# Kernel tuning notes

Measured on AMD Instinct MI355X. Metric: run time of the kernel, lower is better.

Reference implementation:

```python
import jax, jax.numpy as jnp
import numpy as np

N_NODES = 80000
N_EDGES = 1280000
D_NODE = 128
D_EDGE = 32
HID = 64
OUT = 32
EPS_GEN = 1e-7
EPS_BN = 1e-5


def _lin_init(key, fan_in, fan_out):
    return (jax.random.normal(key, (fan_in, fan_out), jnp.float32) / np.sqrt(fan_in))


def setup_inputs() -> dict:
    key = jax.random.key(0)
    ks = jax.random.split(key, 20)
    inp = {
        "x": jax.random.normal(ks[0], (N_NODES, D_NODE), jnp.float32),
        "edge_index": jax.random.randint(ks[1], (2, N_EDGES), 0, N_NODES, jnp.int32),
        "edge_attr": jax.random.normal(ks[2], (N_EDGES, D_EDGE), jnp.float32),
        # encoders
        "node_W": _lin_init(ks[3], D_NODE, HID), "node_b": jnp.zeros((HID,), jnp.float32),
        "edge_W": _lin_init(ks[4], D_EDGE, HID), "edge_b": jnp.zeros((HID,), jnp.float32),
        # GENConv layer 1 MLP: [HID -> 2HID (bias=False)] -> BN -> ReLU -> [2HID -> HID (bias=False)]
        "c1_W1": _lin_init(ks[5], HID, 2 * HID), "c1_g": jnp.ones((2 * HID,), jnp.float32), "c1_be": jnp.zeros((2 * HID,), jnp.float32), "c1_W2": _lin_init(ks[6], 2 * HID, HID),
        # GENConv layer 2
        "c2_W1": _lin_init(ks[7], HID, 2 * HID), "c2_g": jnp.ones((2 * HID,), jnp.float32), "c2_be": jnp.zeros((2 * HID,), jnp.float32), "c2_W2": _lin_init(ks[8], 2 * HID, HID),
        # edge update linears on concat(3*HID)
        "l1_W": _lin_init(ks[9], 3 * HID, HID), "l1_b": jnp.zeros((HID,), jnp.float32),
        "l2_W": _lin_init(ks[10], 3 * HID, OUT), "l2_b": jnp.zeros((OUT,), jnp.float32),
    }
    return inp


def _scatter_softmax_agg(msg, dst, n_nodes):
    # SoftmaxAggregation with t=1: per-destination, per-feature softmax weights
    m = jax.ops.segment_max(msg, dst, num_segments=n_nodes)  # [N, H]
    m = jnp.where(jnp.isfinite(m), m, 0.0)                   # nodes w/o in-edges
    ex = jnp.exp(msg - m[dst])                               # [E, H]
    denom = jax.ops.segment_sum(ex, dst, num_segments=n_nodes)
    alpha = ex / (denom[dst] + 1e-16)
    return jax.ops.segment_sum(msg * alpha, dst, num_segments=n_nodes)


def _batchnorm(h, gamma, beta):
    mu = jnp.mean(h, axis=0)
    var = jnp.var(h, axis=0)
    return (h - mu) * jax.lax.rsqrt(var + EPS_BN) * gamma + beta


def _genconv(x, src, dst, edge_attr, W1, g, be, W2):
    msg = jax.nn.relu(x[src] + edge_attr) + EPS_GEN          # [E, HID]
    agg = _scatter_softmax_agg(msg, dst, x.shape[0])         # [N, HID]
    h = agg + x
    h = jax.nn.relu(_batchnorm(h @ W1, g, be))
    return h @ W2


def reference(x, edge_index, edge_attr, node_W, node_b, edge_W, edge_b,
              c1_W1, c1_g, c1_be, c1_W2, c2_W1, c2_g, c2_be, c2_W2,
              l1_W, l1_b, l2_W, l2_b):
    src, dst = edge_index[0], edge_index[1]
    ea = edge_attr @ edge_W + edge_b                          # [E, HID]
    h = x @ node_W + node_b                                   # [N, HID]

    convs = [(c1_W1, c1_g, c1_be, c1_W2), (c2_W1, c2_g, c2_be, c2_W2)]
    lins = [(l1_W, l1_b), (l2_W, l2_b)]
    for (W1, g, be, W2), (lW, lb) in zip(convs, lins):
        h = jax.nn.relu(_genconv(h, src, dst, ea, W1, g, be, W2))
        # dropout is identity in eval mode
        ef = jnp.concatenate([h[src], ea, h[dst]], axis=-1)   # [E, 3*HID]
        ea = ef @ lW + lb
    return h, ea
```

## Files before the change

### kernel.cpp

```cpp
#include <hip/hip_runtime.h>
#include <hip/hip_bf16.h>

#define N_NODES 80000
#define N_EDGES 1280000
constexpr int DN = 128;
constexpr int DE = 32;
constexpr int H  = 64;
constexpr int H2 = 128;
constexpr int CSTRIDE = 32;
constexpr float EPS_GEN = 1e-7f;
constexpr float EPS_BN  = 1e-5f;

typedef _Float16 f16x8 __attribute__((ext_vector_type(8)));
typedef _Float16 f16x4 __attribute__((ext_vector_type(4)));
typedef float f32x4 __attribute__((ext_vector_type(4)));

__device__ __forceinline__ void atomAddF(float* p, float v) {
  __hip_atomic_fetch_add(p, v, __ATOMIC_RELAXED, __HIP_MEMORY_SCOPE_AGENT);
}

struct PrepDesc { const float* W; _Float16* img; int K; int OC; int blkStart; };
struct PrepAll { PrepDesc d[8]; };

__global__ void k_prep_all(PrepAll P) {
  int b = blockIdx.x;
  int i = 0;
#pragma unroll
  for (int t = 1; t < 8; ++t)
    if (P.d[t].blkStart <= b) i = t;
  const PrepDesc D = P.d[i];
  int idx = (b - D.blkStart) * 256 + threadIdx.x;
  if (idx >= D.K * D.OC) return;
  int nslabK = D.K >> 5;
  int j = idx & 7, m16 = (idx >> 3) & 15, kg = (idx >> 7) & 3;
  int slab = idx >> 9;
  int kk = slab % nslabK, n2 = slab / nslabK;
  int k = kk * 32 + kg * 8 + j, n = n2 * 16 + m16;
  D.img[idx] = (_Float16)D.W[k * D.OC + n];
}

template <int K, int OC, bool IN16, bool AFFINE, bool BIAS,
          bool RELU_OUT, bool OUT16, bool OUT32, bool SCATOUT, bool STATS>
__global__ __launch_bounds__(256) void k_dense(
    const void* __restrict__ Ain, const _Float16* __restrict__ wimg,
    const float* __restrict__ bias, const float* __restrict__ sums,
    const float* __restrict__ g, const float* __restrict__ be,
    const int* __restrict__ posmap,
    _Float16* __restrict__ out16, float* __restrict__ out32,
    float* __restrict__ sums_out) {
  constexpr int NK = K / 32, NF = OC / 16;
  __shared__ float sSC[AFFINE ? H2 : 1], sSH[AFFINE ? H2 : 1];
  __shared__ float sStat[STATS ? 1024 : 1];
  const int tid = threadIdx.x, wv = tid >> 6, lane = tid & 63;
  const int m16 = lane & 15, kg = lane >> 4;
  const int rowbase = blockIdx.x * 64 + wv * 16;
  if constexpr (AFFINE) {
    for (int i = tid; i < H2; i += 256) {
      float mu  = sums[i] * (1.0f / N_NODES);
      float var = sums[H2 + i] * (1.0f / N_NODES) - mu * mu;
      float sc  = rsqrtf(var + EPS_BN) * g[i];
      sSC[i] = sc;
      sSH[i] = be[i] - mu * sc;
    }
    __syncthreads();
  }
  const int arow = rowbase + m16;
  f32x4 acc[NF];
#pragma unroll
  for (int n2 = 0; n2 < NF; ++n2) {
    float bv = BIAS ? bias[n2 * 16 + m16] : 0.0f;
    acc[n2] = (f32x4){bv, bv, bv, bv};
  }
  const _Float16* wp = wimg + (size_t)lane * 8;
#pragma unroll
  for (int kk = 0; kk < NK; ++kk) {
    f16x8 a;
    if constexpr (IN16) {
      const _Float16* ap = (const _Float16*)Ain + (size_t)arow * K + kg * 8 + kk * 32;
      a = *(const f16x8*)ap;
      if constexpr (AFFINE) {
#pragma unroll
        for (int j = 0; j < 8; ++j) {
          int f = kg * 8 + kk * 32 + j;
          float v = fmaxf(fmaf((float)a[j], sSC[f], sSH[f]), 0.0f);
          a[j] = (_Float16)v;
        }
      }
    } else {
      const float* ap = (const float*)Ain + (size_t)arow * K + kg * 8 + kk * 32;
      float4 v0 = *(const float4*)ap;
      float4 v1 = *(const float4*)(ap + 4);
      a = (f16x8){(_Float16)v0.x, (_Float16)v0.y, (_Float16)v0.z, (_Float16)v0.w,
                  (_Float16)v1.x, (_Float16)v1.y, (_Float16)v1.z, (_Float16)v1.w};
    }
#pragma unroll
    for (int n2 = 0; n2 < NF; ++n2) {
      f16x8 bb = *(const f16x8*)(wp + ((size_t)(n2 * NK + kk) << 9));
      acc[n2] = __builtin_amdgcn_mfma_f32_16x16x32_f16(a, bb, acc[n2], 0, 0, 0);
    }
  }
#pragma unroll
  for (int n2 = 0; n2 < NF; ++n2)
#pragma unroll
    for (int r = 0; r < 4; ++r) {
      float o = acc[n2][r];
      if constexpr (RELU_OUT) o = fmaxf(o, 0.0f);
      int orow = rowbase + kg * 4 + r;
      if constexpr (SCATOUT) orow = posmap[orow];
      size_t oi = (size_t)orow * OC + n2 * 16 + m16;
      if constexpr (OUT16) out16[oi] = (_Float16)o;
      if constexpr (OUT32) out32[oi] = o;
    }
  if constexpr (STATS) {
    static_assert(!STATS || NF == 8, "STATS assumes OC==128");
#pragma unroll
    for (int n2 = 0; n2 < NF; ++n2) {
      float s = acc[n2][0] + acc[n2][1] + acc[n2][2] + acc[n2][3];
      float q = acc[n2][0] * acc[n2][0] + acc[n2][1] * acc[n2][1] +
                acc[n2][2] * acc[n2][2] + acc[n2][3] * acc[n2][3];
      s += __shfl_xor(s, 16); s += __shfl_xor(s, 32);
      q += __shfl_xor(q, 16); q += __shfl_xor(q, 32);
      if (kg == 0) {
        sStat[wv * 128 + n2 * 16 + m16] = s;
        sStat[512 + wv * 128 + n2 * 16 + m16] = q;
      }
    }
    __syncthreads();
    {
      int which = tid >> 7, f = tid & 127;
      const float* b0 = sStat + which * 512;
      float v = b0[f] + b0[128 + f] + b0[256 + f] + b0[384 + f];
      atomAddF(&sums_out[which * H2 + f], v);
    }
  }
}

template <int OC, typename OUT_T, int T, bool SCAT>
__global__ __launch_bounds__(256) void k_edge_upd_srt(
    const _Float16* __restrict__ h, const _Float16* __restrict__ ea,
    const int4* __restrict__ eidsQ,
    const _Float16* __restrict__ wimg, const float* __restrict__ lb,
    OUT_T* __restrict__ eout) {
  constexpr int NF = OC / 16;
  __shared__ _Float16 sWf[NF * 6 * 512];
  __shared__ int sS[T * 64], sD[T * 64];
  __shared__ int sE[SCAT ? T * 64 : 1];
  const int tid = threadIdx.x, wv = tid >> 6, lane = tid & 63;
  const int m16 = lane & 15, kg = lane >> 4;
  const int p0 = blockIdx.x * (T * 64);

  for (int i = tid; i < T * 64; i += 256) {
    int4 t = eidsQ[p0 + i];
    sS[i] = t.y;
    sD[i] = t.z;
    if constexpr (SCAT) sE[i] = t.x;
  }
  {
    const float4* s4 = (const float4*)wimg;
    float4* d4 = (float4*)sWf;
    constexpr int NV = NF * 6 * 512 / 8;
    for (int i = tid; i < NV; i += 256) d4[i] = s4[i];
  }
  __syncthreads();
  const _Float16* wp = sWf + (size_t)lane * 8;

  float bias_[NF];
#pragma unroll
  for (int n2 = 0; n2 < NF; ++n2) bias_[n2] = lb[n2 * 16 + m16];

  f16x8 FA[6], FB[6];
  auto LOADA = [&](f16x8* F, int l) {
    const _Float16* a0 = h + (size_t)sS[l] * H + kg * 8;
    const _Float16* a1 = ea + (size_t)(p0 + l) * H + kg * 8;
    const _Float16* a2 = h + (size_t)sD[l] * H + kg * 8;
    F[0] = *(const f16x8*)a0;
    F[1] = *(const f16x8*)(a0 + 32);
    F[2] = *(const f16x8*)a1;
    F[3] = *(const f16x8*)(a1 + 32);
    F[4] = *(const f16x8*)a2;
    F[5] = *(const f16x8*)(a2 + 32);
  };
  auto COMPUTE = [&](const f16x8* F, int l) {
    f32x4 acc[NF];
#pragma unroll
    for (int n2 = 0; n2 < NF; ++n2)
      acc[n2] = (f32x4){bias_[n2], bias_[n2], bias_[n2], bias_[n2]};
#pragma unroll
    for (int kk = 0; kk < 6; ++kk)
#pragma unroll
      for (int n2 = 0; n2 < NF; ++n2) {
        f16x8 bb = *(const f16x8*)(wp + ((n2 * 6 + kk) << 9));
        acc[n2] = __builtin_amdgcn_mfma_f32_16x16x32_f16(F[kk], bb, acc[n2], 0, 0, 0);
      }
    const int lbase = l - m16;
#pragma unroll
    for (int n2 = 0; n2 < NF; ++n2)
#pragma unroll
      for (int r = 0; r < 4; ++r) {
        int lr = lbase + kg * 4 + r;
        int col = n2 * 16 + m16;
        if constexpr (SCAT)
          eout[(size_t)sE[lr] * OC + col] = (OUT_T)acc[n2][r];
        else
          eout[(size_t)(p0 + lr) * OC + col] = (OUT_T)acc[n2][r];
      }
  };

  const int l0 = wv * 16 + m16;
  LOADA(FA, l0);
  if (T > 1) LOADA(FB, l0 + 64);
#pragma unroll
  for (int t = 0; t < T; ++t) {
    if (t & 1) {
      COMPUTE(FB, l0 + t * 64);
      if (t + 2 < T) LOADA(FB, l0 + (t + 2) * 64);
    } else {
      COMPUTE(FA, l0 + t * 64);
      if (t + 2 < T) LOADA(FA, l0 + (t + 2) * 64);
    }
  }
}

__global__ void k_rank(const int* __restrict__ dst, int* cntPad, int* __restrict__ rank) {
  int e = blockIdx.x * blockDim.x + threadIdx.x;
  if (e < N_EDGES)
    rank[e] = atomicAdd(&cntPad[(size_t)dst[e] * CSTRIDE], 1);
}

__global__ void k_scan_blk(const int* __restrict__ cntPad, int* __restrict__ bsum) {
  __shared__ int sh[256];
  int i = blockIdx.x * 256 + threadIdx.x;
  sh[threadIdx.x] = (i < N_NODES) ? cntPad[(size_t)i * CSTRIDE] : 0;
  __syncthreads();
  for (int s = 128; s > 0; s >>= 1) {
    if (threadIdx.x < s) sh[threadIdx.x] += sh[threadIdx.x + s];
    __syncthreads();
  }
  if (threadIdx.x == 0) bsum[blockIdx.x] = sh[0];
}

__global__ void k_scan_top(int* bsum, int nb) {
  __shared__ int sh[512];
  int t = threadIdx.x;
  int orig = (t < nb) ? bsum[t] : 0;
  sh[t] = orig;
  __syncthreads();
  for (int off = 1; off < 512; off <<= 1) {
    int v = (t >= off) ? sh[t - off] : 0;
    __syncthreads();
    sh[t] += v;
    __syncthreads();
  }
  if (t < nb) bsum[t] = sh[t] - orig;
}

__global__ void k_scan_fin(const int* __restrict__ cntPad, const int* __restrict__ bsum,
                           int* __restrict__ start, int* __restrict__ cntC) {
  __shared__ int sh[256];
  int i = blockIdx.x * 256 + threadIdx.x;
  int t = threadIdx.x;
  int orig = (i < N_NODES) ? cntPad[(size_t)i * CSTRIDE] : 0;
  sh[t] = orig;
  __syncthreads();
  for (int off = 1; off < 256; off <<= 1) {
    int v = (t >= off) ? sh[t - off] : 0;
    __syncthreads();
    sh[t] += v;
    __syncthreads();
  }
  if (i < N_NODES) {
    start[i] = bsum[blockIdx.x] + sh[t] - orig;
    cntC[i] = orig;
  }
}

__global__ void k_scatter(const int* __restrict__ src, const int* __restrict__ dst,
                          const int* __restrict__ rank, const int* __restrict__ start,
                          int4* __restrict__ eidsQ, int* __restrict__ posOf) {
  int e = blockIdx.x * blockDim.x + threadIdx.x;
  if (e < N_EDGES) {
    int d = dst[e];
    int pos = start[d] + rank[e];
    eidsQ[pos] = make_int4(e, src[e], d, 0);
    posOf[e] = pos;
  }
}

__global__ __launch_bounds__(256) void k_agg_csr(
    const _Float16* __restrict__ h, const _Float16* __restrict__ ea_s,
    const int4* __restrict__ eidsQ, const int* __restrict__ start,
    const int* __restrict__ cnt, _Float16* __restrict__ hsum,
    float* __restrict__ sums_clr) {
  if (blockIdx.x == 0) sums_clr[threadIdx.x] = 0.0f;
  const int lane = threadIdx.x & 63;
  const int wid  = (int)((blockIdx.x * blockDim.x + threadIdx.x) >> 6);
  if (wid >= N_NODES) return;
  const int ep = lane >> 3, fg = lane & 7;
  const int s0 = start[wid], c = cnt[wid];
  float num[8] = {0.f, 0.f, 0.f, 0.f, 0.f, 0.f, 0.f, 0.f};
  float den[8] = {0.f, 0.f, 0.f, 0.f, 0.f, 0.f, 0.f, 0.f};
  if (c > 0) {
    const int nit = (c + 7) >> 3;
    int idx = min(ep, c - 1);
    int2 pe = *(const int2*)(eidsQ + s0 + idx);
    f16x8 hA = *(const f16x8*)(h + (size_t)pe.y * H + fg * 8);
    f16x8 eA = *(const f16x8*)(ea_s + (size_t)(s0 + idx) * H + fg * 8);
    bool vA = (ep < c);
    f16x8 hB = hA, eB = eA;
    bool vB = false;
    if (nit > 1) {
      idx = min(8 + ep, c - 1);
      pe = *(const int2*)(eidsQ + s0 + idx);
      hB = *(const f16x8*)(h + (size_t)pe.y * H + fg * 8);
      eB = *(const f16x8*)(ea_s + (size_t)(s0 + idx) * H + fg * 8);
      vB = (8 + ep < c);
    }
    for (int i = 0; i < nit; ++i) {
      f16x8 hc = hA, ec = eA;
      bool vc = vA;
      hA = hB; eA = eB; vA = vB;
      if (i + 2 < nit) {
        idx = min((i + 2) * 8 + ep, c - 1);
        pe = *(const int2*)(eidsQ + s0 + idx);
        hB = *(const f16x8*)(h + (size_t)pe.y * H + fg * 8);
        eB = *(const f16x8*)(ea_s + (size_t)(s0 + idx) * H + fg * 8);
        vB = ((i + 2) * 8 + ep < c);
      }
#pragma unroll
      for (int j = 0; j < 8; ++j) {
        float m = fmaxf((float)hc[j] + (float)ec[j], 0.0f) + EPS_GEN;
        float ex = vc ? __expf(m) : 0.0f;
        num[j] = fmaf(m, ex, num[j]);
        den[j] += ex;
      }
    }
  }
#pragma unroll
  for (int j = 0; j < 8; ++j) {
    num[j] += __shfl_xor(num[j], 8);
    num[j] += __shfl_xor(num[j], 16);
    num[j] += __shfl_xor(num[j], 32);
    den[j] += __shfl_xor(den[j], 8);
    den[j] += __shfl_xor(den[j], 16);
    den[j] += __shfl_xor(den[j], 32);
  }
  if (ep == 0) {
    f16x8 hs = *(const f16x8*)(h + (size_t)wid * H + fg * 8);
    f16x8 o;
#pragma unroll
    for (int j = 0; j < 8; ++j)
      o[j] = (_Float16)(num[j] / (den[j] + 1e-16f) + (float)hs[j]);
    *(f16x8*)(hsum + (size_t)wid * H + fg * 8) = o;
  }
}

extern "C" void kernel_launch(void* const* d_in, const int* in_sizes, int n_in,
                              void* d_out, int out_size, void* d_ws, size_t ws_size,
                              hipStream_t stream) {
  (void)in_sizes; (void)n_in; (void)out_size; (void)ws_size;
  const float* x      = (const float*)d_in[0];
  const int*   eidx   = (const int*)d_in[1];
  const float* eattr  = (const float*)d_in[2];
  const float* node_W = (const float*)d_in[3];
  const float* node_b = (const float*)d_in[4];
  const float* edge_W = (const float*)d_in[5];
  const float* edge_b = (const float*)d_in[6];
  const float* c1_W1  = (const float*)d_in[7];
  const float* c1_g   = (const float*)d_in[8];
  const float* c1_be  = (const float*)d_in[9];
  const float* c1_W2  = (const float*)d_in[10];
  const float* c2_W1  = (const float*)d_in[11];
  const float* c2_g   = (const float*)d_in[12];
  const float* c2_be  = (const float*)d_in[13];
  const float* c2_W2  = (const float*)d_in[14];
  const float* l1_W   = (const float*)d_in[15];
  const float* l1_b   = (const float*)d_in[16];
  const float* l2_W   = (const float*)d_in[17];
  const float* l2_b   = (const float*)d_in[18];

  const int* src = eidx;
  const int* dst = eidx + N_EDGES;

  char* wsb = (char*)d_ws;
  size_t off = 0;
  _Float16* ea_s  = (_Float16*)(wsb + off); off += (size_t)N_EDGES * H * 2;
  _Float16* hA16  = (_Float16*)(wsb + off); off += (size_t)N_NODES * H * 2;
  _Float16* hB16  = (_Float16*)(wsb + off); off += (size_t)N_NODES * H * 2;
  _Float16* hC16  = (_Float16*)(wsb + off); off += (size_t)N_NODES * H * 2;
  _Float16* hsum16= (_Float16*)(wsb + off); off += (size_t)N_NODES * H * 2;
  _Float16* h3    = (_Float16*)(wsb + off); off += (size_t)N_NODES * H2 * 2;
  float* sums     = (float*)(wsb + off);    off += 256 * 4;
  int* cntPad     = (int*)(wsb + off);      off += (size_t)N_NODES * CSTRIDE * 4;
  int* startA     = (int*)(wsb + off);      off += (size_t)N_NODES * 4;
  int* cntC       = (int*)(wsb + off);      off += (size_t)N_NODES * 4;
  int* bsum       = (int*)(wsb + off);      off += 512 * 4;
  int* rankE      = (int*)(wsb + off);      off += (size_t)N_EDGES * 4;
  int4* eidsQ     = (int4*)(wsb + off);     off += (size_t)N_EDGES * 16;
  int* posOf      = (int*)(wsb + off);      off += (size_t)N_EDGES * 4;
  _Float16* wE    = (_Float16*)(wsb + off); off += DE * H * 2;
  _Float16* wN    = (_Float16*)(wsb + off); off += DN * H * 2;
  _Float16* w1a   = (_Float16*)(wsb + off); off += H * H2 * 2;
  _Float16* w1b   = (_Float16*)(wsb + off); off += H * H2 * 2;
  _Float16* w2a   = (_Float16*)(wsb + off); off += H2 * H * 2;
  _Float16* w2b   = (_Float16*)(wsb + off); off += H2 * H * 2;
  _Float16* wL1   = (_Float16*)(wsb + off); off += 3 * H * H * 2;
  _Float16* wL2   = (_Float16*)(wsb + off); off += 3 * H * 32 * 2;

  float* h_out  = (float*)d_out;
  float* ea_out = (float*)d_out + (size_t)N_NODES * H;

  constexpr int NB = (N_NODES + 255) / 256;

  PrepAll P;
  P.d[0] = {edge_W, wE, DE, H, 0};
  P.d[1] = {node_W, wN, DN, H, 8};
  P.d[2] = {c1_W1, w1a, H, H2, 40};
  P.d[3] = {c2_W1, w1b, H, H2, 72};
  P.d[4] = {c1_W2, w2a, H2, H, 104};
  P.d[5] = {c2_W2, w2b, H2, H, 136};
  P.d[6] = {l1_W, wL1, 192, H, 168};
  P.d[7] = {l2_W, wL2, 192, 32, 216};
  k_prep_all<<<240, 256, 0, stream>>>(P);

  hipMemsetAsync(cntPad, 0, (size_t)N_NODES * CSTRIDE * 4, stream);
  k_rank<<<(N_EDGES + 255) / 256, 256, 0, stream>>>(dst, cntPad, rankE);
  k_scan_blk<<<NB, 256, 0, stream>>>(cntPad, bsum);
  k_scan_top<<<1, 512, 0, stream>>>(bsum, NB);
  k_scan_fin<<<NB, 256, 0, stream>>>(cntPad, bsum, startA, cntC);
  k_scatter<<<(N_EDGES + 255) / 256, 256, 0, stream>>>(src, dst, rankE, startA, eidsQ, posOf);

  k_dense<DE, H, false, false, true, false, true, false, true, false>
      <<<N_EDGES / 64, 256, 0, stream>>>(eattr, wE, edge_b, nullptr, nullptr, nullptr,
                                         posOf, ea_s, nullptr, nullptr);
  k_dense<DN, H, false, false, true, false, true, false, false, false>
      <<<N_NODES / 64, 256, 0, stream>>>(x, wN, node_b, nullptr, nullptr, nullptr,
                                         nullptr, hA16, nullptr, nullptr);

  k_agg_csr<<<(N_NODES + 3) / 4, 256, 0, stream>>>(hA16, ea_s, eidsQ, startA, cntC, hsum16, sums);
  k_dense<H, H2, true, false, false, false, true, false, false, true>
      <<<N_NODES / 64, 256, 0, stream>>>(hsum16, w1a, nullptr, nullptr, nullptr, nullptr,
                                         nullptr, h3, nullptr, sums);
  k_dense<H2, H, true, true, false, true, true, false, false, false>
      <<<N_NODES / 64, 256, 0, stream>>>(h3, w2a, nullptr, sums, c1_g, c1_be,
                                         nullptr, hB16, nullptr, nullptr);
  k_edge_upd_srt<64, _Float16, 16, false>
      <<<N_EDGES / 1024, 256, 0, stream>>>(hB16, ea_s, eidsQ, wL1, l1_b, ea_s);

  k_agg_csr<<<(N_NODES + 3) / 4, 256, 0, stream>>>(hB16, ea_s, eidsQ, startA, cntC, hsum16, sums);
  k_dense<H, H2, true, false, false, false, true, false, false, true>
      <<<N_NODES / 64, 256, 0, stream>>>(hsum16, w1b, nullptr, nullptr, nullptr, nullptr,
                                         nullptr, h3, nullptr, sums);
  k_dense<H2, H, true, true, false, true, true, true, false, false>
      <<<N_NODES / 64, 256, 0, stream>>>(h3, w2b, nullptr, sums, c2_g, c2_be,
                                         nullptr, hC16, h_out, nullptr);
  k_edge_upd_srt<32, float, 16, true>
      <<<N_EDGES / 1024, 256, 0, stream>>>(hC16, ea_s, eidsQ, wL2, l2_b, ea_out);
}
```

Before: 602.3 us.

## Recompute first MLP matmul in fused BN+second-matmul kernel to drop h3 buffer

The first node-MLP matmul pass now only computes batch-norm statistics and no longer writes the 80000x128 fp16 intermediate. A new fused kernel recomputes that matmul, applies BN scale/shift and ReLU in registers, stages the tile in shared memory, and runs the second matmul directly. This trades a small amount of redundant MFMA work for removing the write and re-read of the intermediate activation.

```diff
diff --git a/kernel.cpp b/kernel.cpp
--- a/kernel.cpp
+++ b/kernel.cpp
@@ -39,31 +39,19 @@
   D.img[idx] = (_Float16)D.W[k * D.OC + n];
 }
 
-template <int K, int OC, bool IN16, bool AFFINE, bool BIAS,
+template <int K, int OC, bool IN16, bool BIAS,
           bool RELU_OUT, bool OUT16, bool OUT32, bool SCATOUT, bool STATS>
 __global__ __launch_bounds__(256) void k_dense(
     const void* __restrict__ Ain, const _Float16* __restrict__ wimg,
-    const float* __restrict__ bias, const float* __restrict__ sums,
-    const float* __restrict__ g, const float* __restrict__ be,
+    const float* __restrict__ bias,
     const int* __restrict__ posmap,
     _Float16* __restrict__ out16, float* __restrict__ out32,
     float* __restrict__ sums_out) {
   constexpr int NK = K / 32, NF = OC / 16;
-  __shared__ float sSC[AFFINE ? H2 : 1], sSH[AFFINE ? H2 : 1];
   __shared__ float sStat[STATS ? 1024 : 1];
   const int tid = threadIdx.x, wv = tid >> 6, lane = tid & 63;
   const int m16 = lane & 15, kg = lane >> 4;
   const int rowbase = blockIdx.x * 64 + wv * 16;
-  if constexpr (AFFINE) {
-    for (int i = tid; i < H2; i += 256) {
-      float mu  = sums[i] * (1.0f / N_NODES);
-      float var = sums[H2 + i] * (1.0f / N_NODES) - mu * mu;
-      float sc  = rsqrtf(var + EPS_BN) * g[i];
-      sSC[i] = sc;
-      sSH[i] = be[i] - mu * sc;
-    }
-    __syncthreads();
-  }
   const int arow = rowbase + m16;
   f32x4 acc[NF];
 #pragma unroll
@@ -78,14 +66,6 @@
     if constexpr (IN16) {
       const _Float16* ap = (const _Float16*)Ain + (size_t)arow * K + kg * 8 + kk * 32;
       a = *(const f16x8*)ap;
-      if constexpr (AFFINE) {
-#pragma unroll
-        for (int j = 0; j < 8; ++j) {
-          int f = kg * 8 + kk * 32 + j;
-          float v = fmaxf(fmaf((float)a[j], sSC[f], sSH[f]), 0.0f);
-          a[j] = (_Float16)v;
-        }
-      }
     } else {
       const float* ap = (const float*)Ain + (size_t)arow * K + kg * 8 + kk * 32;
       float4 v0 = *(const float4*)ap;
@@ -99,18 +79,20 @@
       acc[n2] = __builtin_amdgcn_mfma_f32_16x16x32_f16(a, bb, acc[n2], 0, 0, 0);
     }
   }
-#pragma unroll
-  for (int n2 = 0; n2 < NF; ++n2)
-#pragma unroll
-    for (int r = 0; r < 4; ++r) {
-      float o = acc[n2][r];
-      if constexpr (RELU_OUT) o = fmaxf(o, 0.0f);
-      int orow = rowbase + kg * 4 + r;
-      if constexpr (SCATOUT) orow = posmap[orow];
-      size_t oi = (size_t)orow * OC + n2 * 16 + m16;
-      if constexpr (OUT16) out16[oi] = (_Float16)o;
-      if constexpr (OUT32) out32[oi] = o;
-    }
+  if constexpr (OUT16 || OUT32) {
+#pragma unroll
+    for (int n2 = 0; n2 < NF; ++n2)
+#pragma unroll
+      for (int r = 0; r < 4; ++r) {
+        float o = acc[n2][r];
+        if constexpr (RELU_OUT) o = fmaxf(o, 0.0f);
+        int orow = rowbase + kg * 4 + r;
+        if constexpr (SCATOUT) orow = posmap[orow];
+        size_t oi = (size_t)orow * OC + n2 * 16 + m16;
+        if constexpr (OUT16) out16[oi] = (_Float16)o;
+        if constexpr (OUT32) out32[oi] = o;
+      }
+  }
   if constexpr (STATS) {
     static_assert(!STATS || NF == 8, "STATS assumes OC==128");
 #pragma unroll
@@ -133,6 +115,76 @@
       atomAddF(&sums_out[which * H2 + f], v);
     }
   }
+}
+
+template <bool OUT32>
+__global__ __launch_bounds__(256) void k_mlp2f(
+    const _Float16* __restrict__ hsum, const _Float16* __restrict__ w1img,
+    const _Float16* __restrict__ w2img, const float* __restrict__ sums,
+    const float* __restrict__ g, const float* __restrict__ be,
+    _Float16* __restrict__ out16, float* __restrict__ out32) {
+  constexpr int TP = 136;
+  __shared__ float sSC[H2], sSH[H2];
+  __shared__ _Float16 sT[64 * TP];
+  const int tid = threadIdx.x, wv = tid >> 6, lane = tid & 63;
+  const int m16 = lane & 15, kg = lane >> 4;
+  const int rowbase = blockIdx.x * 64 + wv * 16;
+
+  for (int i = tid; i < H2; i += 256) {
+    float mu  = sums[i] * (1.0f / N_NODES);
+    float var = sums[H2 + i] * (1.0f / N_NODES) - mu * mu;
+    float sc  = rsqrtf(var + EPS_BN) * g[i];
+    sSC[i] = sc;
+    sSH[i] = be[i] - mu * sc;
+  }
+
+  f32x4 acc1[8];
+#pragma unroll
+  for (int n2 = 0; n2 < 8; ++n2) acc1[n2] = (f32x4){0.f, 0.f, 0.f, 0.f};
+  const _Float16* wp1 = w1img + (size_t)lane * 8;
+#pragma unroll
+  for (int kk = 0; kk < 2; ++kk) {
+    f16x8 a = *(const f16x8*)(hsum + (size_t)(rowbase + m16) * H + kg * 8 + kk * 32);
+#pragma unroll
+    for (int n2 = 0; n2 < 8; ++n2) {
+      f16x8 bb = *(const f16x8*)(wp1 + ((size_t)(n2 * 2 + kk) << 9));
+      acc1[n2] = __builtin_amdgcn_mfma_f32_16x16x32_f16(a, bb, acc1[n2], 0, 0, 0);
+    }
+  }
+  __syncthreads();
+#pragma unroll
+  for (int n2 = 0; n2 < 8; ++n2) {
+    int col = n2 * 16 + m16;
+    float sc = sSC[col], sh = sSH[col];
+#pragma unroll
+    for (int r = 0; r < 4; ++r) {
+      float v = fmaxf(fmaf(acc1[n2][r], sc, sh), 0.0f);
+      sT[(wv * 16 + kg * 4 + r) * TP + col] = (_Float16)v;
+    }
+  }
+  __syncthreads();
+  f32x4 acc2[4];
+#pragma unroll
+  for (int n2 = 0; n2 < 4; ++n2) acc2[n2] = (f32x4){0.f, 0.f, 0.f, 0.f};
+  const _Float16* wp2 = w2img + (size_t)lane * 8;
+#pragma unroll
+  for (int kk = 0; kk < 4; ++kk) {
+    f16x8 a2 = *(const f16x8*)&sT[(wv * 16 + m16) * TP + kg * 8 + kk * 32];
+#pragma unroll
+    for (int n2 = 0; n2 < 4; ++n2) {
+      f16x8 bb = *(const f16x8*)(wp2 + ((size_t)(n2 * 4 + kk) << 9));
+      acc2[n2] = __builtin_amdgcn_mfma_f32_16x16x32_f16(a2, bb, acc2[n2], 0, 0, 0);
+    }
+  }
+#pragma unroll
+  for (int n2 = 0; n2 < 4; ++n2)
+#pragma unroll
+    for (int r = 0; r < 4; ++r) {
+      float o = fmaxf(acc2[n2][r], 0.0f);
+      size_t oi = (size_t)(rowbase + kg * 4 + r) * H + n2 * 16 + m16;
+      out16[oi] = (_Float16)o;
+      if constexpr (OUT32) out32[oi] = o;
+    }
 }
 
 template <int OC, typename OUT_T, int T, bool SCAT>
@@ -388,7 +440,6 @@
   _Float16* hB16  = (_Float16*)(wsb + off); off += (size_t)N_NODES * H * 2;
   _Float16* hC16  = (_Float16*)(wsb + off); off += (size_t)N_NODES * H * 2;
   _Float16* hsum16= (_Float16*)(wsb + off); off += (size_t)N_NODES * H * 2;
-  _Float16* h3    = (_Float16*)(wsb + off); off += (size_t)N_NODES * H2 * 2;
   float* sums     = (float*)(wsb + off);    off += 256 * 4;
   int* cntPad     = (int*)(wsb + off);      off += (size_t)N_NODES * CSTRIDE * 4;
   int* startA     = (int*)(wsb + off);      off += (size_t)N_NODES * 4;
@@ -429,30 +480,28 @@
   k_scan_fin<<<NB, 256, 0, stream>>>(cntPad, bsum, startA, cntC);
   k_scatter<<<(N_EDGES + 255) / 256, 256, 0, stream>>>(src, dst, rankE, startA, eidsQ, posOf);
 
-  k_dense<DE, H, false, false, true, false, true, false, true, false>
-      <<<N_EDGES / 64, 256, 0, stream>>>(eattr, wE, edge_b, nullptr, nullptr, nullptr,
+  k_dense<DE, H, false, true, false, true, false, true, false>
+      <<<N_EDGES / 64, 256, 0, stream>>>(eattr, wE, edge_b,
                                          posOf, ea_s, nullptr, nullptr);
-  k_dense<DN, H, false, false, true, false, true, false, false, false>
-      <<<N_NODES / 64, 256, 0, stream>>>(x, wN, node_b, nullptr, nullptr, nullptr,
+  k_dense<DN, H, false, true, false, true, false, false, false>
+      <<<N_NODES / 64, 256, 0, stream>>>(x, wN, node_b,
                                          nullptr, hA16, nullptr, nullptr);
 
   k_agg_csr<<<(N_NODES + 3) / 4, 256, 0, stream>>>(hA16, ea_s, eidsQ, startA, cntC, hsum16, sums);
-  k_dense<H, H2, true, false, false, false, true, false, false, true>
-      <<<N_NODES / 64, 256, 0, stream>>>(hsum16, w1a, nullptr, nullptr, nullptr, nullptr,
-                                         nullptr, h3, nullptr, sums);
-  k_dense<H2, H, true, true, false, true, true, false, false, false>
-      <<<N_NODES / 64, 256, 0, stream>>>(h3, w2a, nullptr, sums, c1_g, c1_be,
-                                         nullptr, hB16, nullptr, nullptr);
+  k_dense<H, H2, true, false, false, false, false, false, true>
+      <<<N_NODES / 64, 256, 0, stream>>>(hsum16, w1a, nullptr,
+                                         nullptr, nullptr, nullptr, sums);
+  k_mlp2f<false><<<N_NODES / 64, 256, 0, stream>>>(hsum16, w1a, w2a, sums,
+                                                   c1_g, c1_be, hB16, nullptr);
   k_edge_upd_srt<64, _Float16, 16, false>
       <<<N_EDGES / 1024, 256, 0, stream>>>(hB16, ea_s, eidsQ, wL1, l1_b, ea_s);
 
   k_agg_csr<<<(N_NODES + 3) / 4, 256, 0, stream>>>(hB16, ea_s, eidsQ, startA, cntC, hsum16, sums);
-  k_dense<H, H2, true, false, false, false, true, false, false, true>
-      <<<N_NODES / 64, 256, 0, stream>>>(hsum16, w1b, nullptr, nullptr, nullptr, nullptr,
-                                         nullptr, h3, nullptr, sums);
-  k_dense<H2, H, true, true, false, true, true, true, false, false>
-      <<<N_NODES / 64, 256, 0, stream>>>(h3, w2b, nullptr, sums, c2_g, c2_be,
-                                         nullptr, hC16, h_out, nullptr);
+  k_dense<H, H2, true, false, false, false, false, false, true>
+      <<<N_NODES / 64, 256, 0, stream>>>(hsum16, w1b, nullptr,
+                                         nullptr, nullptr, nullptr, sums);
+  k_mlp2f<true><<<N_NODES / 64, 256, 0, stream>>>(hsum16, w1b, w2b, sums,
+                                                  c2_g, c2_be, hC16, h_out);
   k_edge_upd_srt<32, float, 16, true>
       <<<N_EDGES / 1024, 256, 0, stream>>>(hC16, ea_s, eidsQ, wL2, l2_b, ea_out);
 }
```

Result: no change. 594.1 us (-1.4%).
